# Kernel tuning notes

Measured on AMD Instinct MI355X. Metric: run time of the kernel, lower is better.

Reference implementation:

```python
import jax, jax.numpy as jnp
import numpy as np

NUM_EDGES = 800_000
NUM_VERTICES = 100_000
NNZ = 1_600_000
D_MODEL = 128


def setup_inputs() -> dict:
    key = jax.random.key(0)
    ks = jax.random.split(key, 10)
    d = D_MODEL
    return {
        "x_e": jax.random.normal(ks[0], (NUM_EDGES, d), dtype=jnp.float32),
        "h_v": jax.random.normal(ks[1], (NUM_VERTICES, d), dtype=jnp.float32),
        "c_v": jax.random.normal(ks[2], (NUM_VERTICES, d), dtype=jnp.float32),
        "W_ih": jax.random.normal(ks[3], (4 * d, d), dtype=jnp.float32) * 0.05,
        "W_hh": jax.random.normal(ks[4], (4 * d, d), dtype=jnp.float32) * 0.05,
        "b_ih": jax.random.normal(ks[5], (4 * d,), dtype=jnp.float32) * 0.05,
        "b_hh": jax.random.normal(ks[6], (4 * d,), dtype=jnp.float32) * 0.05,
        "nnz_edge_ids": jax.random.randint(ks[7], (NNZ,), 0, NUM_EDGES, dtype=jnp.int32),
        "nnz_vertex_ids": jax.random.randint(ks[8], (NNZ,), 0, NUM_VERTICES, dtype=jnp.int32),
        "v_batch": jax.random.randint(ks[9], (NUM_VERTICES,), 0, 8, dtype=jnp.int32),
    }


def reference(x_e, h_v, c_v, W_ih, W_hh, b_ih, b_hh, nnz_edge_ids, nnz_vertex_ids, v_batch):
    # msg = adj_t.T @ x_e : scatter-add edge embeddings into incident vertices
    msg = jax.ops.segment_sum(x_e[nnz_edge_ids], nnz_vertex_ids,
                              num_segments=h_v.shape[0])  # [V, d]
    # single-step LSTM update (PyTorch gate order: i, f, g, o)
    gates = msg @ W_ih.T + b_ih + h_v @ W_hh.T + b_hh  # [V, 4d]
    i, f, g, o = jnp.split(gates, 4, axis=-1)
    i = jax.nn.sigmoid(i)
    f = jax.nn.sigmoid(f)
    g = jnp.tanh(g)
    o = jax.nn.sigmoid(o)
    c_new = f * c_v + i * g
    h_new = o * jnp.tanh(c_new)
    return (h_new, c_new)
```

## Files before the change

### kernel.cpp

```cpp
#include <hip/hip_runtime.h>
#include <hip/hip_bf16.h>

#define NE 800000
#define NV 100000
#define NNZN 1600000
#define D 128
#define NB_SCAN 98

typedef short short8 __attribute__((ext_vector_type(8)));
typedef short s16x4 __attribute__((ext_vector_type(4)));
typedef float f32x4 __attribute__((ext_vector_type(4)));
typedef float f32x2 __attribute__((ext_vector_type(2)));

__device__ __forceinline__ unsigned short f2bfu(float f) {
  union { float f; unsigned u; } x;
  x.f = f;
  unsigned u = x.u;
  u += ((u >> 16) & 1u) + 0x7FFFu;
  return (unsigned short)(u >> 16);
}

__device__ __forceinline__ float fsigmoid(float x) {
  return 1.0f / (1.0f + __expf(-x));
}
__device__ __forceinline__ float ftanh(float x) {
  return 2.0f / (1.0f + __expf(-2.0f * x)) - 1.0f;
}

__global__ __launch_bounds__(256) void wconv_kernel(
    const float* __restrict__ W_ih, const float* __restrict__ W_hh,
    const float* __restrict__ b_ih, const float* __restrict__ b_hh,
    short* __restrict__ Wcat, float* __restrict__ bcomb,
    int* __restrict__ counts) {
  int idx = blockIdx.x * 256 + threadIdx.x;
  int n = idx >> 8;
  int k = idx & 255;
  float val = (k < 128) ? W_ih[n * 128 + k] : W_hh[n * 128 + (k - 128)];
  Wcat[idx] = (short)f2bfu(val);
  if (idx < 512) bcomb[idx] = b_ih[idx] + b_hh[idx];
  if (idx < NV) counts[idx] = 0;
}

__global__ __launch_bounds__(256) void hist_kernel(
    const int* __restrict__ vid, int* __restrict__ counts) {
  int j = blockIdx.x * 256 + threadIdx.x;
  if (j < NNZN) atomicAdd(&counts[vid[j]], 1);
}

__global__ __launch_bounds__(256) void scan1_kernel(
    const int* __restrict__ counts, int* __restrict__ offs, int* __restrict__ bsums) {
  __shared__ int lds[256];
  const int t = threadIdx.x;
  const int base = blockIdx.x * 1024 + t * 4;
  int c[4];
  int s = 0;
#pragma unroll
  for (int i = 0; i < 4; ++i) {
    int idx = base + i;
    c[i] = (idx < NV) ? counts[idx] : 0;
    s += c[i];
  }
  lds[t] = s;
  __syncthreads();
  for (int off = 1; off < 256; off <<= 1) {
    int v = (t >= off) ? lds[t - off] : 0;
    __syncthreads();
    lds[t] += v;
    __syncthreads();
  }
  if (t == 255) bsums[blockIdx.x] = lds[255];
  int run = lds[t] - s;
#pragma unroll
  for (int i = 0; i < 4; ++i) {
    int idx = base + i;
    if (idx < NV) offs[idx] = run;
    run += c[i];
  }
}

__global__ __launch_bounds__(256) void scan2_kernel(int* __restrict__ bsums) {
  __shared__ int lds[256];
  const int t = threadIdx.x;
  int v = (t < NB_SCAN) ? bsums[t] : 0;
  lds[t] = v;
  __syncthreads();
  for (int off = 1; off < 256; off <<= 1) {
    int x = (t >= off) ? lds[t - off] : 0;
    __syncthreads();
    lds[t] += x;
    __syncthreads();
  }
  if (t < NB_SCAN) bsums[t] = lds[t] - v;
}

__global__ __launch_bounds__(256) void scan3_kernel(
    int* __restrict__ offs, const int* __restrict__ bsums) {
  const int base = blockIdx.x * 1024 + threadIdx.x * 4;
  const int add = bsums[blockIdx.x];
#pragma unroll
  for (int i = 0; i < 4; ++i) {
    int idx = base + i;
    if (idx < NV) offs[idx] += add;
  }
}

__global__ __launch_bounds__(256) void scatter_perm_kernel(
    const int* __restrict__ eid, const int* __restrict__ vid,
    int* __restrict__ offs, int* __restrict__ perm) {
  int j = blockIdx.x * 256 + threadIdx.x;
  if (j < NNZN) {
    int v = vid[j];
    int pos = atomicAdd(&offs[v], 1);
    perm[pos] = eid[j];
  }
}

__global__ __launch_bounds__(256) void gather_kernel(
    const float* __restrict__ x_e, const int* __restrict__ ends,
    const int* __restrict__ counts, const int* __restrict__ perm,
    unsigned short* __restrict__ msg) {
  const int wv = (blockIdx.x * 256 + threadIdx.x) >> 6;
  const int lane = threadIdx.x & 63;
  const int half = lane >> 5;
  const int pos = lane & 31;
  if (wv >= NV) return;
  const int deg = counts[wv];
  const int start = ends[wv] - deg;
  f32x4 a0 = {0.f, 0.f, 0.f, 0.f}, a1 = a0, a2 = a0, a3 = a0;
  int i = half;
  for (; i + 6 < deg; i += 8) {
    int e0 = perm[start + i];
    int e1 = perm[start + i + 2];
    int e2 = perm[start + i + 4];
    int e3 = perm[start + i + 6];
    a0 += *(const f32x4*)(x_e + (size_t)e0 * D + pos * 4);
    a1 += *(const f32x4*)(x_e + (size_t)e1 * D + pos * 4);
    a2 += *(const f32x4*)(x_e + (size_t)e2 * D + pos * 4);
    a3 += *(const f32x4*)(x_e + (size_t)e3 * D + pos * 4);
  }
  for (; i < deg; i += 2) {
    int e = perm[start + i];
    a0 += *(const f32x4*)(x_e + (size_t)e * D + pos * 4);
  }
  a0 += a1;
  a2 += a3;
  a0 += a2;
  f32x4 b;
  b[0] = __shfl_xor(a0[0], 32);
  b[1] = __shfl_xor(a0[1], 32);
  b[2] = __shfl_xor(a0[2], 32);
  b[3] = __shfl_xor(a0[3], 32);
  a0 += b;
  if (half == 0) {
    s16x4 p;
    p[0] = (short)f2bfu(a0[0]);
    p[1] = (short)f2bfu(a0[1]);
    p[2] = (short)f2bfu(a0[2]);
    p[3] = (short)f2bfu(a0[3]);
    *(s16x4*)(msg + (size_t)wv * D + pos * 4) = p;
  }
}

__global__ __launch_bounds__(256) void lstm_kernel(
    const unsigned short* __restrict__ msg, const float* __restrict__ h_v,
    const float* __restrict__ c_v, const short* __restrict__ Wcat,
    const float* __restrict__ bcomb, float* __restrict__ out) {
  __shared__ char Atile[32 * 256 * 2];
  const int tid = threadIdx.x;
  const int vbase = blockIdx.x * 32;

#pragma unroll
  for (int i = 0; i < 4; ++i) {
    int cid = tid + i * 256;
    int row = cid >> 5;
    int c = cid & 31;
    short8 v;
    if (c < 16) {
      v = *(const short8*)(msg + (size_t)(vbase + row) * D + c * 8);
    } else {
      const float* src = h_v + (size_t)(vbase + row) * D + (c - 16) * 8;
      f32x4 a = *(const f32x4*)(src);
      f32x4 b = *(const f32x4*)(src + 4);
      v[0] = (short)f2bfu(a[0]); v[1] = (short)f2bfu(a[1]);
      v[2] = (short)f2bfu(a[2]); v[3] = (short)f2bfu(a[3]);
      v[4] = (short)f2bfu(b[0]); v[5] = (short)f2bfu(b[1]);
      v[6] = (short)f2bfu(b[2]); v[7] = (short)f2bfu(b[3]);
    }
    int byteoff = row * 512 + c * 16;
    byteoff ^= (row & 7) << 4;
    *(short8*)(Atile + byteoff) = v;
  }
  __syncthreads();

  const int wid = tid >> 6;
  const int lane = tid & 63;
  const int l16 = lane & 15;
  const int lhi = lane >> 4;

  f32x4 acc[2][4][2] = {};

#pragma unroll
  for (int kk = 0; kk < 8; ++kk) {
    short8 afrag[2];
#pragma unroll
    for (int m = 0; m < 2; ++m) {
      int row = m * 16 + l16;
      int byteoff = row * 512 + kk * 64 + lhi * 16;
      byteoff ^= (row & 7) << 4;
      afrag[m] = *(const short8*)(Atile + byteoff);
    }
#pragma unroll
    for (int g = 0; g < 4; ++g) {
#pragma unroll
      for (int t = 0; t < 2; ++t) {
        int n0 = g * 128 + wid * 32 + t * 16;
        short8 bfrag = *(const short8*)(Wcat + (size_t)(n0 + l16) * 256 + kk * 32 + lhi * 8);
        acc[0][g][t] = __builtin_amdgcn_mfma_f32_16x16x32_bf16(afrag[0], bfrag, acc[0][g][t], 0, 0, 0);
        acc[1][g][t] = __builtin_amdgcn_mfma_f32_16x16x32_bf16(afrag[1], bfrag, acc[1][g][t], 0, 0, 0);
      }
    }
  }

  float* out_h = out;
  float* out_c = out + (size_t)NV * D;
#pragma unroll
  for (int m = 0; m < 2; ++m) {
#pragma unroll
    for (int t = 0; t < 2; ++t) {
      int d = wid * 32 + t * 16 + l16;
      float bi = bcomb[d];
      float bf = bcomb[128 + d];
      float bg = bcomb[256 + d];
      float bo = bcomb[384 + d];
#pragma unroll
      for (int r = 0; r < 4; ++r) {
        int v = vbase + m * 16 + lhi * 4 + r;
        float gi = acc[m][0][t][r] + bi;
        float gf = acc[m][1][t][r] + bf;
        float gg = acc[m][2][t][r] + bg;
        float go = acc[m][3][t][r] + bo;
        float ii = fsigmoid(gi);
        float ff = fsigmoid(gf);
        float g_ = ftanh(gg);
        float oo = fsigmoid(go);
        float cv = c_v[(size_t)v * D + d];
        float cn = ff * cv + ii * g_;
        float hn = oo * ftanh(cn);
        out_h[(size_t)v * D + d] = hn;
        out_c[(size_t)v * D + d] = cn;
      }
    }
  }
}

extern "C" void kernel_launch(void* const* d_in, const int* in_sizes, int n_in,
                              void* d_out, int out_size, void* d_ws, size_t ws_size,
                              hipStream_t stream) {
  const float* x_e  = (const float*)d_in[0];
  const float* h_v  = (const float*)d_in[1];
  const float* c_v  = (const float*)d_in[2];
  const float* W_ih = (const float*)d_in[3];
  const float* W_hh = (const float*)d_in[4];
  const float* b_ih = (const float*)d_in[5];
  const float* b_hh = (const float*)d_in[6];
  const int* eid    = (const int*)d_in[7];
  const int* vid    = (const int*)d_in[8];
  float* out = (float*)d_out;

  char* w = (char*)d_ws;
  short* Wcat  = (short*)w;                 w += 512 * 256 * sizeof(short);
  float* bcomb = (float*)w;                 w += 512 * sizeof(float);
  int* counts  = (int*)w;                   w += NV * sizeof(int);
  int* offs    = (int*)w;                   w += NV * sizeof(int);
  int* bsums   = (int*)w;                   w += 128 * sizeof(int);
  int* perm    = (int*)w;                   w += NNZN * sizeof(int);
  unsigned short* msg = (unsigned short*)w;

  wconv_kernel<<<512, 256, 0, stream>>>(W_ih, W_hh, b_ih, b_hh, Wcat, bcomb, counts);
  hist_kernel<<<(NNZN + 255) / 256, 256, 0, stream>>>(vid, counts);
  scan1_kernel<<<NB_SCAN, 256, 0, stream>>>(counts, offs, bsums);
  scan2_kernel<<<1, 256, 0, stream>>>(bsums);
  scan3_kernel<<<NB_SCAN, 256, 0, stream>>>(offs, bsums);
  scatter_perm_kernel<<<(NNZN + 255) / 256, 256, 0, stream>>>(eid, vid, offs, perm);
  gather_kernel<<<(NV + 3) / 4, 256, 0, stream>>>(x_e, offs, counts, perm, msg);
  lstm_kernel<<<NV / 32, 256, 0, stream>>>(msg, h_v, c_v, Wcat, bcomb, out);
}
```

Baseline: 500.4 us.

## Fuse gather into LSTM kernel and pre-swizzle weights into MFMA fragment order

The segment-sum gather now runs inside the LSTM GEMM kernel: each wave accumulates 8 vertex rows and writes the bf16 message straight into the shared A tile, so the intermediate msg buffer and one launch go away. The weight conversion kernel now lays Wcat out in per-wave, per-kk fragment order so each B-fragment load is contiguous. The catch is less gather parallelism per block: each wave handles 8 vertices serially, which could lower memory-level parallelism for the latency-bound random x_e reads.

```diff
diff --git a/kernel.cpp b/kernel.cpp
--- a/kernel.cpp
+++ b/kernel.cpp
@@ -33,10 +33,26 @@
     short* __restrict__ Wcat, float* __restrict__ bcomb,
     int* __restrict__ counts) {
   int idx = blockIdx.x * 256 + threadIdx.x;
-  int n = idx >> 8;
-  int k = idx & 255;
-  float val = (k < 128) ? W_ih[n * 128 + k] : W_hh[n * 128 + (k - 128)];
-  Wcat[idx] = (short)f2bfu(val);
+  if (idx < 16384) {
+    int c8 = idx;
+    int pos = c8 & 63;
+    int t   = (c8 >> 6) & 1;
+    int g   = (c8 >> 7) & 3;
+    int kk  = (c8 >> 9) & 7;
+    int wid = (c8 >> 12) & 3;
+    int n = g * 128 + wid * 32 + t * 16 + (pos >> 2);
+    int k0 = kk * 32 + (pos & 3) * 8;
+    const float* src = (k0 < 128) ? (W_ih + (size_t)n * 128 + k0)
+                                  : (W_hh + (size_t)n * 128 + (k0 - 128));
+    f32x4 a = *(const f32x4*)(src);
+    f32x4 b = *(const f32x4*)(src + 4);
+    short8 v;
+    v[0] = (short)f2bfu(a[0]); v[1] = (short)f2bfu(a[1]);
+    v[2] = (short)f2bfu(a[2]); v[3] = (short)f2bfu(a[3]);
+    v[4] = (short)f2bfu(b[0]); v[5] = (short)f2bfu(b[1]);
+    v[6] = (short)f2bfu(b[2]); v[7] = (short)f2bfu(b[3]);
+    *(short8*)(Wcat + (size_t)c8 * 8) = v;
+  }
   if (idx < 512) bcomb[idx] = b_ih[idx] + b_hh[idx];
   if (idx < NV) counts[idx] = 0;
 }
@@ -115,85 +131,80 @@
   }
 }
 
-__global__ __launch_bounds__(256) void gather_kernel(
+__global__ __launch_bounds__(256) void fused_kernel(
     const float* __restrict__ x_e, const int* __restrict__ ends,
     const int* __restrict__ counts, const int* __restrict__ perm,
-    unsigned short* __restrict__ msg) {
-  const int wv = (blockIdx.x * 256 + threadIdx.x) >> 6;
-  const int lane = threadIdx.x & 63;
-  const int half = lane >> 5;
-  const int pos = lane & 31;
-  if (wv >= NV) return;
-  const int deg = counts[wv];
-  const int start = ends[wv] - deg;
-  f32x4 a0 = {0.f, 0.f, 0.f, 0.f}, a1 = a0, a2 = a0, a3 = a0;
-  int i = half;
-  for (; i + 6 < deg; i += 8) {
-    int e0 = perm[start + i];
-    int e1 = perm[start + i + 2];
-    int e2 = perm[start + i + 4];
-    int e3 = perm[start + i + 6];
-    a0 += *(const f32x4*)(x_e + (size_t)e0 * D + pos * 4);
-    a1 += *(const f32x4*)(x_e + (size_t)e1 * D + pos * 4);
-    a2 += *(const f32x4*)(x_e + (size_t)e2 * D + pos * 4);
-    a3 += *(const f32x4*)(x_e + (size_t)e3 * D + pos * 4);
-  }
-  for (; i < deg; i += 2) {
-    int e = perm[start + i];
-    a0 += *(const f32x4*)(x_e + (size_t)e * D + pos * 4);
-  }
-  a0 += a1;
-  a2 += a3;
-  a0 += a2;
-  f32x4 b;
-  b[0] = __shfl_xor(a0[0], 32);
-  b[1] = __shfl_xor(a0[1], 32);
-  b[2] = __shfl_xor(a0[2], 32);
-  b[3] = __shfl_xor(a0[3], 32);
-  a0 += b;
-  if (half == 0) {
-    s16x4 p;
-    p[0] = (short)f2bfu(a0[0]);
-    p[1] = (short)f2bfu(a0[1]);
-    p[2] = (short)f2bfu(a0[2]);
-    p[3] = (short)f2bfu(a0[3]);
-    *(s16x4*)(msg + (size_t)wv * D + pos * 4) = p;
-  }
-}
-
-__global__ __launch_bounds__(256) void lstm_kernel(
-    const unsigned short* __restrict__ msg, const float* __restrict__ h_v,
-    const float* __restrict__ c_v, const short* __restrict__ Wcat,
-    const float* __restrict__ bcomb, float* __restrict__ out) {
+    const float* __restrict__ h_v, const float* __restrict__ c_v,
+    const short* __restrict__ Wcat, const float* __restrict__ bcomb,
+    float* __restrict__ out) {
   __shared__ char Atile[32 * 256 * 2];
   const int tid = threadIdx.x;
   const int vbase = blockIdx.x * 32;
-
-#pragma unroll
-  for (int i = 0; i < 4; ++i) {
-    int cid = tid + i * 256;
-    int row = cid >> 5;
-    int c = cid & 31;
-    short8 v;
-    if (c < 16) {
-      v = *(const short8*)(msg + (size_t)(vbase + row) * D + c * 8);
-    } else {
-      const float* src = h_v + (size_t)(vbase + row) * D + (c - 16) * 8;
-      f32x4 a = *(const f32x4*)(src);
-      f32x4 b = *(const f32x4*)(src + 4);
-      v[0] = (short)f2bfu(a[0]); v[1] = (short)f2bfu(a[1]);
-      v[2] = (short)f2bfu(a[2]); v[3] = (short)f2bfu(a[3]);
-      v[4] = (short)f2bfu(b[0]); v[5] = (short)f2bfu(b[1]);
-      v[6] = (short)f2bfu(b[2]); v[7] = (short)f2bfu(b[3]);
-    }
-    int byteoff = row * 512 + c * 16;
-    byteoff ^= (row & 7) << 4;
-    *(short8*)(Atile + byteoff) = v;
-  }
-  __syncthreads();
-
   const int wid = tid >> 6;
   const int lane = tid & 63;
+  const int half = lane >> 5;
+  const int pos = lane & 31;
+
+#pragma unroll
+  for (int i = 0; i < 2; ++i) {
+    int cid = tid + i * 256;
+    int row = cid >> 4;
+    int c = 16 + (cid & 15);
+    const float* src = h_v + (size_t)(vbase + row) * D + (c - 16) * 8;
+    f32x4 a = *(const f32x4*)(src);
+    f32x4 b = *(const f32x4*)(src + 4);
+    short8 v;
+    v[0] = (short)f2bfu(a[0]); v[1] = (short)f2bfu(a[1]);
+    v[2] = (short)f2bfu(a[2]); v[3] = (short)f2bfu(a[3]);
+    v[4] = (short)f2bfu(b[0]); v[5] = (short)f2bfu(b[1]);
+    v[6] = (short)f2bfu(b[2]); v[7] = (short)f2bfu(b[3]);
+    int byteoff = (row * 512 + c * 16) ^ ((row & 7) << 4);
+    *(short8*)(Atile + byteoff) = v;
+  }
+
+#pragma unroll 1
+  for (int s = 0; s < 8; ++s) {
+    const int row = wid * 8 + s;
+    const int v = vbase + row;
+    const int deg = counts[v];
+    const int start = ends[v] - deg;
+    f32x4 a0 = {0.f, 0.f, 0.f, 0.f}, a1 = a0, a2 = a0, a3 = a0;
+    int i = half;
+    for (; i + 6 < deg; i += 8) {
+      int e0 = perm[start + i];
+      int e1 = perm[start + i + 2];
+      int e2 = perm[start + i + 4];
+      int e3 = perm[start + i + 6];
+      a0 += *(const f32x4*)(x_e + (size_t)e0 * D + pos * 4);
+      a1 += *(const f32x4*)(x_e + (size_t)e1 * D + pos * 4);
+      a2 += *(const f32x4*)(x_e + (size_t)e2 * D + pos * 4);
+      a3 += *(const f32x4*)(x_e + (size_t)e3 * D + pos * 4);
+    }
+    for (; i < deg; i += 2) {
+      int e = perm[start + i];
+      a0 += *(const f32x4*)(x_e + (size_t)e * D + pos * 4);
+    }
+    a0 += a1;
+    a2 += a3;
+    a0 += a2;
+    f32x4 b;
+    b[0] = __shfl_xor(a0[0], 32);
+    b[1] = __shfl_xor(a0[1], 32);
+    b[2] = __shfl_xor(a0[2], 32);
+    b[3] = __shfl_xor(a0[3], 32);
+    a0 += b;
+    if (half == 0) {
+      s16x4 p;
+      p[0] = (short)f2bfu(a0[0]);
+      p[1] = (short)f2bfu(a0[1]);
+      p[2] = (short)f2bfu(a0[2]);
+      p[3] = (short)f2bfu(a0[3]);
+      int byteoff = (row * 512 + pos * 8) ^ ((row & 7) << 4);
+      *(s16x4*)(Atile + byteoff) = p;
+    }
+  }
+  __syncthreads();
+
   const int l16 = lane & 15;
   const int lhi = lane >> 4;
 
@@ -205,16 +216,16 @@
 #pragma unroll
     for (int m = 0; m < 2; ++m) {
       int row = m * 16 + l16;
-      int byteoff = row * 512 + kk * 64 + lhi * 16;
-      byteoff ^= (row & 7) << 4;
+      int byteoff = (row * 512 + kk * 64 + lhi * 16) ^ ((row & 7) << 4);
       afrag[m] = *(const short8*)(Atile + byteoff);
     }
 #pragma unroll
     for (int g = 0; g < 4; ++g) {
 #pragma unroll
       for (int t = 0; t < 2; ++t) {
-        int n0 = g * 128 + wid * 32 + t * 16;
-        short8 bfrag = *(const short8*)(Wcat + (size_t)(n0 + l16) * 256 + kk * 32 + lhi * 8);
+        size_t boff = (size_t)(wid * 64 + kk * 8 + g * 2 + t) * 1024
+                    + (size_t)(l16 * 4 + lhi) * 16;
+        short8 bfrag = *(const short8*)((const char*)Wcat + boff);
         acc[0][g][t] = __builtin_amdgcn_mfma_f32_16x16x32_bf16(afrag[0], bfrag, acc[0][g][t], 0, 0, 0);
         acc[1][g][t] = __builtin_amdgcn_mfma_f32_16x16x32_bf16(afrag[1], bfrag, acc[1][g][t], 0, 0, 0);
       }
@@ -273,8 +284,7 @@
   int* counts  = (int*)w;                   w += NV * sizeof(int);
   int* offs    = (int*)w;                   w += NV * sizeof(int);
   int* bsums   = (int*)w;                   w += 128 * sizeof(int);
-  int* perm    = (int*)w;                   w += NNZN * sizeof(int);
-  unsigned short* msg = (unsigned short*)w;
+  int* perm    = (int*)w;
 
   wconv_kernel<<<512, 256, 0, stream>>>(W_ih, W_hh, b_ih, b_hh, Wcat, bcomb, counts);
   hist_kernel<<<(NNZN + 255) / 256, 256, 0, stream>>>(vid, counts);
@@ -282,6 +292,5 @@
   scan2_kernel<<<1, 256, 0, stream>>>(bsums);
   scan3_kernel<<<NB_SCAN, 256, 0, stream>>>(offs, bsums);
   scatter_perm_kernel<<<(NNZN + 255) / 256, 256, 0, stream>>>(eid, vid, offs, perm);
-  gather_kernel<<<(NV + 3) / 4, 256, 0, stream>>>(x_e, offs, counts, perm, msg);
-  lstm_kernel<<<NV / 32, 256, 0, stream>>>(msg, h_v, c_v, Wcat, bcomb, out);
-}
+  fused_kernel<<<NV / 32, 256, 0, stream>>>(x_e, offs, counts, perm, h_v, c_v, Wcat, bcomb, out);
+}
```

New measurement: 503.8 us. Within noise of the previous version (+0.7%).
